# Kernel tuning notes

Hardware: AMD Instinct MI355X
Metric: run time of the kernel (lower is better)

Reference implementation:

```python
import jax, jax.numpy as jnp
import numpy as np

AMP = 2  # from init_kwargs

def setup_inputs() -> dict:
    key = jax.random.key(0)
    k1, k2 = jax.random.split(key)
    B, C, H, W = 4, 32, 256, 256
    x_q = jax.random.normal(k1, (B, C, H, W), dtype=jnp.float32)
    x_k = jax.random.normal(k2, (B, C, H, W), dtype=jnp.float32)
    return {"x_q": x_q, "x_k": x_k, "num_heads": 4}


def reference(x_q, x_k, num_heads):
    amp = AMP
    ks = 2 * amp + 1  # kernel_size
    B, C, H, W = x_q.shape
    head_dim = C // num_heads
    scale = head_dim ** (-0.5)
    # (B, head_dim, heads, H, W)
    q = x_q.reshape(B, head_dim, num_heads, H, W) * scale
    k = x_k.reshape(B, head_dim, num_heads, H, W)
    k_pad = jnp.pad(k, ((0, 0), (0, 0), (0, 0), (amp, amp), (amp, amp)))
    # validity mask: padded region is invalid (mask < 0.5 in original)
    valid = jnp.pad(jnp.ones((H, W), dtype=x_q.dtype), ((amp, amp), (amp, amp)))
    attn = []
    for i in range(ks):  # static loop over 25 offsets
        for j in range(ks):
            # per-offset dot product over head_dim -> (B, heads, H, W)
            a = jnp.sum(q * k_pad[:, :, :, i:i + H, j:j + W], axis=1)
            a = jnp.where(valid[i:i + H, j:j + W] > 0.5, a, jnp.asarray(-1000.0, a.dtype))
            attn.append(a)
    attn = jnp.stack(attn, axis=1)          # (B, ks*ks, heads, H, W)
    attn = jax.nn.softmax(attn, axis=1)
    # offset grid: arange(-s//2+1, s//2+1) == [-amp, ..., amp]
    offs = jnp.arange(-amp, amp + 1, dtype=x_q.dtype)
    grid = jnp.stack(jnp.meshgrid(offs, offs, indexing='ij'), axis=-1).reshape(ks * ks, 2)
    # offset-weighted sum over the ks*ks window positions -> (B, 2, heads, H, W)
    v_ = jnp.einsum('bkhxy,kc->bchxy', attn, grid)
    # mean over heads -> (B, 2, H, W)
    return jnp.mean(v_, axis=2)
```

## Files before the change

### kernel.cpp

```cpp
#include <hip/hip_runtime.h>

#define Bdim 4
#define Cdim 32
#define NH   4
#define HD   8
#define Hdim 256
#define Wdim 256
#define AMP  2
#define KS   5

#define XT    32
#define TY    8
#define TROWS (TY + 2*AMP)
#define TCOLS (XT + 8)
#define TILE_F (Cdim * TROWS * TCOLS)
#define TILE_F4 (TILE_F / 4)

__global__ __launch_bounds__(256) void natt_offset_kernel(
    const float* __restrict__ xq,
    const float* __restrict__ xk,
    float* __restrict__ out)
{
    __shared__ float kt[TILE_F];

    const int tid = threadIdx.x;
    const int bid = blockIdx.x;
    const int r8  = bid & 7;
    const int u   = bid >> 3;
    const int yt  = r8 * 4 + (u & 3);
    const int rst = u >> 2;
    const int xt  = rst & 7;
    const int b   = rst >> 3;

    const int Y0 = yt * TY;
    const int X0 = xt * XT;

    const int h   = tid >> 6;
    const int s   = tid & 63;
    const int row = s >> 3;
    const int qx  = s & 7;

    const int y  = Y0 + row;
    const int x0 = X0 + qx * 4;

    const size_t plane = (size_t)Hdim * Wdim;
    const float scale = 0.35355339059327373f;

    {
        const float* kb = xk + (size_t)b * Cdim * plane;
        #pragma unroll
        for (int it = 0; it < TILE_F4 / 256; ++it) {
            const int i   = tid + it * 256;
            const int ch  = i / (TROWS * (TCOLS / 4));
            const int rem = i % (TROWS * (TCOLS / 4));
            const int rw  = rem / (TCOLS / 4);
            const int q4  = rem % (TCOLS / 4);
            int yr = Y0 - AMP + rw;
            yr = yr < 0 ? 0 : (yr > Hdim - 1 ? Hdim - 1 : yr);
            int xc = X0 - 4 + q4 * 4;
            xc = xc < 0 ? 0 : (xc > Wdim - 4 ? Wdim - 4 : xc);
            const float4 v = *(const float4*)(kb + (size_t)ch * plane + (size_t)yr * Wdim + xc);
            *(float4*)(kt + ch * (TROWS * TCOLS) + rw * TCOLS + q4 * 4) = v;
        }
    }

    const float* qb = xq + (size_t)b * Cdim * plane + (size_t)y * Wdim + x0;
    float q[HD][4];
    #pragma unroll
    for (int d = 0; d < HD; ++d) {
        const float4 qv = *(const float4*)(qb + (size_t)(d * NH + h) * plane);
        q[d][0] = qv.x * scale; q[d][1] = qv.y * scale;
        q[d][2] = qv.z * scale; q[d][3] = qv.w * scale;
    }

    __syncthreads();

    float Z[4]  = {0.f, 0.f, 0.f, 0.f};
    float sx[4] = {0.f, 0.f, 0.f, 0.f};
    float sy[4] = {0.f, 0.f, 0.f, 0.f};

    const float* ktb = kt + (size_t)(row) * TCOLS + qx * 4;

    #pragma unroll
    for (int r = 0; r < KS; ++r) {
        float dot[KS][4];
        #pragma unroll
        for (int dj = 0; dj < KS; ++dj) {
            dot[dj][0] = 0.f; dot[dj][1] = 0.f; dot[dj][2] = 0.f; dot[dj][3] = 0.f;
        }

        #pragma unroll
        for (int d = 0; d < HD; ++d) {
            const float* wp = ktb + (size_t)(d * NH + h) * (TROWS * TCOLS) + r * TCOLS;
            const float4 w0 = *(const float4*)(wp);
            const float4 w1 = *(const float4*)(wp + 4);
            const float4 w2 = *(const float4*)(wp + 8);
            const float w[12] = {w0.x, w0.y, w0.z, w0.w,
                                 w1.x, w1.y, w1.z, w1.w,
                                 w2.x, w2.y, w2.z, w2.w};
            #pragma unroll
            for (int dj = 0; dj < KS; ++dj) {
                #pragma unroll
                for (int p = 0; p < 4; ++p)
                    dot[dj][p] += q[d][p] * w[p + dj + 2];
            }
        }

        const int yy = y + r - AMP;
        const bool rowok = (yy >= 0) && (yy < Hdim);
        const float fdi = (float)(r - AMP);
        #pragma unroll
        for (int dj = 0; dj < KS; ++dj) {
            const float fdj = (float)(dj - AMP);
            #pragma unroll
            for (int p = 0; p < 4; ++p) {
                const int xx = x0 + p + dj - AMP;
                const bool ok = rowok && (xx >= 0) && (xx < Wdim);
                const float e = ok ? __expf(dot[dj][p]) : 0.f;
                Z[p]  += e;
                sx[p] += e * fdi;
                sy[p] += e * fdj;
            }
        }
    }

    __syncthreads();
    float* red = kt;
    const int pxl = row * XT + qx * 4;
    {
        const float i0 = 1.f / Z[0], i1 = 1.f / Z[1], i2 = 1.f / Z[2], i3 = 1.f / Z[3];
        float4 vx4 = make_float4(sx[0]*i0, sx[1]*i1, sx[2]*i2, sx[3]*i3);
        float4 vy4 = make_float4(sy[0]*i0, sy[1]*i1, sy[2]*i2, sy[3]*i3);
        *(float4*)(red + (h * 2 + 0) * (XT * TY) + pxl) = vx4;
        *(float4*)(red + (h * 2 + 1) * (XT * TY) + pxl) = vy4;
    }
    __syncthreads();

    if (h < 2) {
        float acc[4] = {0.f, 0.f, 0.f, 0.f};
        #pragma unroll
        for (int hh = 0; hh < NH; ++hh) {
            const float4 v = *(const float4*)(red + (hh * 2 + h) * (XT * TY) + pxl);
            acc[0] += v.x; acc[1] += v.y; acc[2] += v.z; acc[3] += v.w;
        }
        float4 o = make_float4(acc[0]*0.25f, acc[1]*0.25f, acc[2]*0.25f, acc[3]*0.25f);
        *(float4*)(out + ((size_t)b * 2 + h) * plane + (size_t)y * Wdim + x0) = o;
    }
}

extern "C" void kernel_launch(void* const* d_in, const int* in_sizes, int n_in,
                              void* d_out, int out_size, void* d_ws, size_t ws_size,
                              hipStream_t stream) {
    const float* xq = (const float*)d_in[0];
    const float* xk = (const float*)d_in[1];
    float* out = (float*)d_out;

    natt_offset_kernel<<<dim3(1024, 1, 1), dim3(256, 1, 1), 0, stream>>>(xq, xk, out);
}
```

Measured before the change: 123.3 us.

## Split per-head work into separate 64-thread blocks with a head-mean pass

Each block now handles a single head with one wavefront, staging only that head's 8 key channels in shared memory. The shared tile shrinks and the grid grows to 4096 blocks, which should raise occupancy and remove the block-level syncs. The cross-head mean moves into a second kernel that reads per-head partials from workspace. This costs an extra launch and a round trip of partial results through global memory, and the key halo loads are no longer shared across heads. The tile row stride also changes to 44.

```diff
diff --git a/kernel.cpp b/kernel.cpp
--- a/kernel.cpp
+++ b/kernel.cpp
@@ -12,36 +12,36 @@
 #define XT    32
 #define TY    8
 #define TROWS (TY + 2*AMP)
-#define TCOLS (XT + 8)
-#define TILE_F (Cdim * TROWS * TCOLS)
-#define TILE_F4 (TILE_F / 4)
+#define TCOLS 44
+#define CH_STRIDE (TROWS * TCOLS)
+#define TILE_F (HD * CH_STRIDE)
 
-__global__ __launch_bounds__(256) void natt_offset_kernel(
+__global__ __launch_bounds__(64) void natt_head_kernel(
     const float* __restrict__ xq,
     const float* __restrict__ xk,
-    float* __restrict__ out)
+    float* __restrict__ part)
 {
     __shared__ float kt[TILE_F];
 
-    const int tid = threadIdx.x;
-    const int bid = blockIdx.x;
-    const int r8  = bid & 7;
+    const int lane = threadIdx.x;
+    const int bid  = blockIdx.x;
+
+    const int xcd = bid & 7;
     const int u   = bid >> 3;
-    const int yt  = r8 * 4 + (u & 3);
-    const int rst = u >> 2;
-    const int xt  = rst & 7;
-    const int b   = rst >> 3;
+    const int yt  = xcd * 4 + (u & 3);
+    const int v   = u >> 2;
+    const int xt  = v & 7;
+    const int w2  = v >> 3;
+    const int h   = w2 & 3;
+    const int b   = w2 >> 2;
 
     const int Y0 = yt * TY;
     const int X0 = xt * XT;
 
-    const int h   = tid >> 6;
-    const int s   = tid & 63;
-    const int row = s >> 3;
-    const int qx  = s & 7;
-
-    const int y  = Y0 + row;
-    const int x0 = X0 + qx * 4;
+    const int row = lane >> 3;
+    const int qx  = lane & 7;
+    const int y   = Y0 + row;
+    const int x0  = X0 + qx * 4;
 
     const size_t plane = (size_t)Hdim * Wdim;
     const float scale = 0.35355339059327373f;
@@ -49,18 +49,19 @@
     {
         const float* kb = xk + (size_t)b * Cdim * plane;
         #pragma unroll
-        for (int it = 0; it < TILE_F4 / 256; ++it) {
-            const int i   = tid + it * 256;
-            const int ch  = i / (TROWS * (TCOLS / 4));
-            const int rem = i % (TROWS * (TCOLS / 4));
-            const int rw  = rem / (TCOLS / 4);
-            const int q4  = rem % (TCOLS / 4);
+        for (int it = 0; it < 15; ++it) {
+            const int i  = lane + it * 64;
+            const int q4 = i % 10;
+            const int t  = i / 10;
+            const int rw = t % 12;
+            const int l  = t / 12;
             int yr = Y0 - AMP + rw;
             yr = yr < 0 ? 0 : (yr > Hdim - 1 ? Hdim - 1 : yr);
             int xc = X0 - 4 + q4 * 4;
             xc = xc < 0 ? 0 : (xc > Wdim - 4 ? Wdim - 4 : xc);
-            const float4 v = *(const float4*)(kb + (size_t)ch * plane + (size_t)yr * Wdim + xc);
-            *(float4*)(kt + ch * (TROWS * TCOLS) + rw * TCOLS + q4 * 4) = v;
+            const float4 kv = *(const float4*)(kb + (size_t)(l * NH + h) * plane
+                                               + (size_t)yr * Wdim + xc);
+            *(float4*)(kt + l * CH_STRIDE + rw * TCOLS + q4 * 4) = kv;
         }
     }
 
@@ -79,7 +80,7 @@
     float sx[4] = {0.f, 0.f, 0.f, 0.f};
     float sy[4] = {0.f, 0.f, 0.f, 0.f};
 
-    const float* ktb = kt + (size_t)(row) * TCOLS + qx * 4;
+    const float* ktb = kt + (size_t)row * TCOLS + qx * 4;
 
     #pragma unroll
     for (int r = 0; r < KS; ++r) {
@@ -91,13 +92,13 @@
 
         #pragma unroll
         for (int d = 0; d < HD; ++d) {
-            const float* wp = ktb + (size_t)(d * NH + h) * (TROWS * TCOLS) + r * TCOLS;
+            const float* wp = ktb + d * CH_STRIDE + r * TCOLS;
             const float4 w0 = *(const float4*)(wp);
             const float4 w1 = *(const float4*)(wp + 4);
-            const float4 w2 = *(const float4*)(wp + 8);
+            const float4 w2v = *(const float4*)(wp + 8);
             const float w[12] = {w0.x, w0.y, w0.z, w0.w,
                                  w1.x, w1.y, w1.z, w1.w,
-                                 w2.x, w2.y, w2.z, w2.w};
+                                 w2v.x, w2v.y, w2v.z, w2v.w};
             #pragma unroll
             for (int dj = 0; dj < KS; ++dj) {
                 #pragma unroll
@@ -124,28 +125,30 @@
         }
     }
 
-    __syncthreads();
-    float* red = kt;
-    const int pxl = row * XT + qx * 4;
-    {
-        const float i0 = 1.f / Z[0], i1 = 1.f / Z[1], i2 = 1.f / Z[2], i3 = 1.f / Z[3];
-        float4 vx4 = make_float4(sx[0]*i0, sx[1]*i1, sx[2]*i2, sx[3]*i3);
-        float4 vy4 = make_float4(sy[0]*i0, sy[1]*i1, sy[2]*i2, sy[3]*i3);
-        *(float4*)(red + (h * 2 + 0) * (XT * TY) + pxl) = vx4;
-        *(float4*)(red + (h * 2 + 1) * (XT * TY) + pxl) = vy4;
-    }
-    __syncthreads();
+    const float i0 = 1.f / Z[0], i1 = 1.f / Z[1], i2 = 1.f / Z[2], i3 = 1.f / Z[3];
+    const size_t pbase = (size_t)((h * Bdim + b) * 2) * plane + (size_t)y * Wdim + x0;
+    *(float4*)(part + pbase)         = make_float4(sx[0]*i0, sx[1]*i1, sx[2]*i2, sx[3]*i3);
+    *(float4*)(part + pbase + plane) = make_float4(sy[0]*i0, sy[1]*i1, sy[2]*i2, sy[3]*i3);
+}
 
-    if (h < 2) {
-        float acc[4] = {0.f, 0.f, 0.f, 0.f};
-        #pragma unroll
-        for (int hh = 0; hh < NH; ++hh) {
-            const float4 v = *(const float4*)(red + (hh * 2 + h) * (XT * TY) + pxl);
-            acc[0] += v.x; acc[1] += v.y; acc[2] += v.z; acc[3] += v.w;
-        }
-        float4 o = make_float4(acc[0]*0.25f, acc[1]*0.25f, acc[2]*0.25f, acc[3]*0.25f);
-        *(float4*)(out + ((size_t)b * 2 + h) * plane + (size_t)y * Wdim + x0) = o;
-    }
+__global__ __launch_bounds__(256) void head_mean_kernel(
+    const float* __restrict__ part,
+    float* __restrict__ out)
+{
+    const int idx = blockIdx.x * 256 + threadIdx.x;
+    const int pq  = (int)(((size_t)Hdim * Wdim) / 4);
+    const int g   = idx / pq;
+    const int r   = idx % pq;
+    const float4* p4 = (const float4*)part;
+    float4 a = p4[(0 * 8 + g) * pq + r];
+    const float4 b1 = p4[(1 * 8 + g) * pq + r];
+    const float4 b2 = p4[(2 * 8 + g) * pq + r];
+    const float4 b3 = p4[(3 * 8 + g) * pq + r];
+    a.x = (a.x + b1.x + b2.x + b3.x) * 0.25f;
+    a.y = (a.y + b1.y + b2.y + b3.y) * 0.25f;
+    a.z = (a.z + b1.z + b2.z + b3.z) * 0.25f;
+    a.w = (a.w + b1.w + b2.w + b3.w) * 0.25f;
+    ((float4*)out)[idx] = a;
 }
 
 extern "C" void kernel_launch(void* const* d_in, const int* in_sizes, int n_in,
@@ -153,7 +156,9 @@
                               hipStream_t stream) {
     const float* xq = (const float*)d_in[0];
     const float* xk = (const float*)d_in[1];
-    float* out = (float*)d_out;
+    float* out  = (float*)d_out;
+    float* part = (float*)d_ws;
 
-    natt_offset_kernel<<<dim3(1024, 1, 1), dim3(256, 1, 1), 0, stream>>>(xq, xk, out);
+    natt_head_kernel<<<dim3(4096, 1, 1), dim3(64, 1, 1), 0, stream>>>(xq, xk, part);
+    head_mean_kernel<<<dim3(512, 1, 1), dim3(256, 1, 1), 0, stream>>>(part, out);
 }
```

Result: slower. 127.9 us (+3.7%).

## Pack key tile as fp16 channel pairs and use fdot2 for dot products

Applied to the files above, without the earlier changes.

The key tile is now stored in shared memory as packed half2 pairs of channels, and q is converted to fp16 pairs. The dot products use v_dot2_f32_f16, which halves LDS footprint and reads and the FMA count. The softmax accumulation is reorganised per pixel so the x-offset weights become a closed-form sum, and launch bounds request 4 blocks per CU for occupancy. The cost is fp16 rounding of q and k, which can shift attention logits and exceed the tolerance.

```diff
diff --git a/kernel.cpp b/kernel.cpp
--- a/kernel.cpp
+++ b/kernel.cpp
@@ -11,17 +11,28 @@
 
 #define XT    32
 #define TY    8
-#define TROWS (TY + 2*AMP)
-#define TCOLS (XT + 8)
-#define TILE_F (Cdim * TROWS * TCOLS)
-#define TILE_F4 (TILE_F / 4)
+#define TROWS 12
+#define TPOS  44
+#define NPAIRS 16
+#define PAIR_STRIDE (TROWS * TPOS)
+#define TILE_SLOTS (NPAIRS * PAIR_STRIDE)
 
-__global__ __launch_bounds__(256) void natt_offset_kernel(
+typedef _Float16 h2 __attribute__((ext_vector_type(2)));
+
+static __device__ __forceinline__ float dot2acc(h2 a, h2 b, float c) {
+#if __has_builtin(__builtin_amdgcn_fdot2)
+    return __builtin_amdgcn_fdot2(a, b, c, false);
+#else
+    return c + (float)a.x * (float)b.x + (float)a.y * (float)b.y;
+#endif
+}
+
+__global__ __launch_bounds__(256, 4) void natt_offset_kernel(
     const float* __restrict__ xq,
     const float* __restrict__ xk,
     float* __restrict__ out)
 {
-    __shared__ float kt[TILE_F];
+    __shared__ __align__(16) float kt[TILE_SLOTS];
 
     const int tid = threadIdx.x;
     const int bid = blockIdx.x;
@@ -35,13 +46,12 @@
     const int Y0 = yt * TY;
     const int X0 = xt * XT;
 
-    const int h   = tid >> 6;
-    const int s   = tid & 63;
-    const int row = s >> 3;
-    const int qx  = s & 7;
-
-    const int y  = Y0 + row;
-    const int x0 = X0 + qx * 4;
+    const int h    = tid >> 6;
+    const int lane = tid & 63;
+    const int row  = lane >> 3;
+    const int qx   = lane & 7;
+    const int y    = Y0 + row;
+    const int x0   = X0 + qx * 4;
 
     const size_t plane = (size_t)Hdim * Wdim;
     const float scale = 0.35355339059327373f;
@@ -49,28 +59,55 @@
     {
         const float* kb = xk + (size_t)b * Cdim * plane;
         #pragma unroll
-        for (int it = 0; it < TILE_F4 / 256; ++it) {
-            const int i   = tid + it * 256;
-            const int ch  = i / (TROWS * (TCOLS / 4));
-            const int rem = i % (TROWS * (TCOLS / 4));
-            const int rw  = rem / (TCOLS / 4);
-            const int q4  = rem % (TCOLS / 4);
-            int yr = Y0 - AMP + rw;
-            yr = yr < 0 ? 0 : (yr > Hdim - 1 ? Hdim - 1 : yr);
-            int xc = X0 - 4 + q4 * 4;
-            xc = xc < 0 ? 0 : (xc > Wdim - 4 ? Wdim - 4 : xc);
-            const float4 v = *(const float4*)(kb + (size_t)ch * plane + (size_t)yr * Wdim + xc);
-            *(float4*)(kt + ch * (TROWS * TCOLS) + rw * TCOLS + q4 * 4) = v;
+        for (int it = 0; it < 8; ++it) {
+            const int j = tid + it * 256;
+            if (j < NPAIRS * TROWS * 10) {
+                const int c4 = j % 10;
+                const int t  = j / 10;
+                const int rw = t % TROWS;
+                const int p2 = t / TROWS;
+                const int hh = p2 & 3;
+                const int d0 = (p2 >> 2) * 2;
+                const int c0 = d0 * NH + hh;
+                int yr = Y0 - AMP + rw;
+                yr = yr < 0 ? 0 : (yr > Hdim - 1 ? Hdim - 1 : yr);
+                const int xs = X0 - 6 + c4 * 4;
+                const int xc = xs < 0 ? 0 : (xs > Wdim - 4 ? Wdim - 4 : xs);
+                const int sh = xs - xc;
+                const float* pa = kb + (size_t)c0 * plane + (size_t)yr * Wdim + xc;
+                const float4 va = *(const float4*)pa;
+                const float4 vb = *(const float4*)(pa + 4 * plane);
+                const float a[4]  = {va.x, va.y, va.z, va.w};
+                const float bb[4] = {vb.x, vb.y, vb.z, vb.w};
+                float o[4];
+                #pragma unroll
+                for (int k2 = 0; k2 < 4; ++k2) {
+                    int idx = k2 + sh;
+                    idx = idx < 0 ? 0 : (idx > 3 ? 3 : idx);
+                    h2 pk;
+                    pk.x = (_Float16)a[idx];
+                    pk.y = (_Float16)bb[idx];
+                    o[k2] = __builtin_bit_cast(float, pk);
+                }
+                *(float4*)(kt + p2 * PAIR_STRIDE + rw * TPOS + c4 * 4) =
+                    make_float4(o[0], o[1], o[2], o[3]);
+            }
         }
     }
 
     const float* qb = xq + (size_t)b * Cdim * plane + (size_t)y * Wdim + x0;
-    float q[HD][4];
+    h2 q2[4][4];
     #pragma unroll
-    for (int d = 0; d < HD; ++d) {
-        const float4 qv = *(const float4*)(qb + (size_t)(d * NH + h) * plane);
-        q[d][0] = qv.x * scale; q[d][1] = qv.y * scale;
-        q[d][2] = qv.z * scale; q[d][3] = qv.w * scale;
+    for (int d2 = 0; d2 < 4; ++d2) {
+        const float4 qa = *(const float4*)(qb + (size_t)((2 * d2)     * NH + h) * plane);
+        const float4 qc = *(const float4*)(qb + (size_t)((2 * d2 + 1) * NH + h) * plane);
+        const float qa4[4] = {qa.x, qa.y, qa.z, qa.w};
+        const float qc4[4] = {qc.x, qc.y, qc.z, qc.w};
+        #pragma unroll
+        for (int p = 0; p < 4; ++p) {
+            q2[d2][p].x = (_Float16)(qa4[p] * scale);
+            q2[d2][p].y = (_Float16)(qc4[p] * scale);
+        }
     }
 
     __syncthreads();
@@ -78,8 +115,6 @@
     float Z[4]  = {0.f, 0.f, 0.f, 0.f};
     float sx[4] = {0.f, 0.f, 0.f, 0.f};
     float sy[4] = {0.f, 0.f, 0.f, 0.f};
-
-    const float* ktb = kt + (size_t)(row) * TCOLS + qx * 4;
 
     #pragma unroll
     for (int r = 0; r < KS; ++r) {
@@ -90,19 +125,20 @@
         }
 
         #pragma unroll
-        for (int d = 0; d < HD; ++d) {
-            const float* wp = ktb + (size_t)(d * NH + h) * (TROWS * TCOLS) + r * TCOLS;
-            const float4 w0 = *(const float4*)(wp);
-            const float4 w1 = *(const float4*)(wp + 4);
-            const float4 w2 = *(const float4*)(wp + 8);
-            const float w[12] = {w0.x, w0.y, w0.z, w0.w,
-                                 w1.x, w1.y, w1.z, w1.w,
-                                 w2.x, w2.y, w2.z, w2.w};
+        for (int d2 = 0; d2 < 4; ++d2) {
+            const float* wp = kt + ((d2 << 2) | h) * PAIR_STRIDE
+                                 + (row + r) * TPOS + (qx * 4 + 4);
+            const float4 wa = *(const float4*)wp;
+            const float4 wb = *(const float4*)(wp + 4);
+            const float wf[8] = {wa.x, wa.y, wa.z, wa.w, wb.x, wb.y, wb.z, wb.w};
+            h2 w[8];
+            #pragma unroll
+            for (int k2 = 0; k2 < 8; ++k2) w[k2] = __builtin_bit_cast(h2, wf[k2]);
             #pragma unroll
             for (int dj = 0; dj < KS; ++dj) {
                 #pragma unroll
                 for (int p = 0; p < 4; ++p)
-                    dot[dj][p] += q[d][p] * w[p + dj + 2];
+                    dot[dj][p] = dot2acc(q2[d2][p], w[p + dj], dot[dj][p]);
             }
         }
 
@@ -110,17 +146,18 @@
         const bool rowok = (yy >= 0) && (yy < Hdim);
         const float fdi = (float)(r - AMP);
         #pragma unroll
-        for (int dj = 0; dj < KS; ++dj) {
-            const float fdj = (float)(dj - AMP);
+        for (int p = 0; p < 4; ++p) {
+            float e[KS];
             #pragma unroll
-            for (int p = 0; p < 4; ++p) {
+            for (int dj = 0; dj < KS; ++dj) {
                 const int xx = x0 + p + dj - AMP;
                 const bool ok = rowok && (xx >= 0) && (xx < Wdim);
-                const float e = ok ? __expf(dot[dj][p]) : 0.f;
-                Z[p]  += e;
-                sx[p] += e * fdi;
-                sy[p] += e * fdj;
+                e[dj] = ok ? __expf(dot[dj][p]) : 0.f;
             }
+            const float er = ((e[0] + e[1]) + (e[2] + e[3])) + e[4];
+            Z[p]  += er;
+            sx[p] += fdi * er;
+            sy[p] += (e[3] - e[1]) + 2.f * (e[4] - e[0]);
         }
     }
 
@@ -129,10 +166,10 @@
     const int pxl = row * XT + qx * 4;
     {
         const float i0 = 1.f / Z[0], i1 = 1.f / Z[1], i2 = 1.f / Z[2], i3 = 1.f / Z[3];
-        float4 vx4 = make_float4(sx[0]*i0, sx[1]*i1, sx[2]*i2, sx[3]*i3);
-        float4 vy4 = make_float4(sy[0]*i0, sy[1]*i1, sy[2]*i2, sy[3]*i3);
-        *(float4*)(red + (h * 2 + 0) * (XT * TY) + pxl) = vx4;
-        *(float4*)(red + (h * 2 + 1) * (XT * TY) + pxl) = vy4;
+        *(float4*)(red + (h * 2 + 0) * (XT * TY) + pxl) =
+            make_float4(sx[0]*i0, sx[1]*i1, sx[2]*i2, sx[3]*i3);
+        *(float4*)(red + (h * 2 + 1) * (XT * TY) + pxl) =
+            make_float4(sy[0]*i0, sy[1]*i1, sy[2]*i2, sy[3]*i3);
     }
     __syncthreads();
 
@@ -143,8 +180,8 @@
             const float4 v = *(const float4*)(red + (hh * 2 + h) * (XT * TY) + pxl);
             acc[0] += v.x; acc[1] += v.y; acc[2] += v.z; acc[3] += v.w;
         }
-        float4 o = make_float4(acc[0]*0.25f, acc[1]*0.25f, acc[2]*0.25f, acc[3]*0.25f);
-        *(float4*)(out + ((size_t)b * 2 + h) * plane + (size_t)y * Wdim + x0) = o;
+        *(float4*)(out + ((size_t)b * 2 + h) * plane + (size_t)y * Wdim + x0) =
+            make_float4(acc[0]*0.25f, acc[1]*0.25f, acc[2]*0.25f, acc[3]*0.25f);
     }
 }
 
```

Measured after the change: 132.5 us. 7.4% more time.
